# Kernel tuning notes

Hardware: AMD Instinct MI355X
Metric: run time of the kernel (lower is better)

## Reference

```python
import jax, jax.numpy as jnp
import numpy as np

W_BIT = 4
G_SIZE = 128
HID = 4096
INTER = 11008
TOKS = (2, 2048)


def _dequant(qw, qz, scales, g_size):
    """Unpack int4 nibbles from int32 and dequantize: (w - zero) * scale.
    qw: [K, N//8] int32, qz: [K//g, N//8] int32, scales: [K//g, N] float.
    Returns dense weight [K, N] in scales.dtype."""
    K = qw.shape[0]
    shifts = (jnp.arange(8, dtype=jnp.int32) * 4)  # 8 nibbles per int32
    w = ((qw[:, :, None] >> shifts) & 0xF).reshape(K, -1).astype(scales.dtype)   # [K, N]
    z = ((qz[:, :, None] >> shifts) & 0xF).reshape(qz.shape[0], -1).astype(scales.dtype)  # [K//g, N]
    zr = jnp.repeat(z, g_size, axis=0)       # broadcast zero-points over group rows
    sr = jnp.repeat(scales, g_size, axis=0)  # broadcast scales over group rows
    return (w - zr) * sr


def setup_inputs() -> dict:
    key = jax.random.key(0)
    ks = jax.random.split(key, 7)
    B, S = TOKS
    x = jax.random.normal(ks[0], (B, S, HID), dtype=jnp.float32)
    imax = 2147483647
    qweight_gu = jax.random.randint(ks[1], (HID, 2 * INTER // 8), 0, imax, dtype=jnp.int32)
    qzeros_gu = jax.random.randint(ks[2], (HID // G_SIZE, 2 * INTER // 8), 0, imax, dtype=jnp.int32)
    scales_gu = jax.random.uniform(ks[3], (HID // G_SIZE, 2 * INTER), dtype=jnp.float32) * 0.01 + 1e-3
    qweight_dn = jax.random.randint(ks[4], (INTER, HID // 8), 0, imax, dtype=jnp.int32)
    qzeros_dn = jax.random.randint(ks[5], (INTER // G_SIZE, HID // 8), 0, imax, dtype=jnp.int32)
    scales_dn = jax.random.uniform(ks[6], (INTER // G_SIZE, HID), dtype=jnp.float32) * 0.01 + 1e-3
    return {"x": x, "qweight_gu": qweight_gu, "qzeros_gu": qzeros_gu, "scales_gu": scales_gu,
            "qweight_dn": qweight_dn, "qzeros_dn": qzeros_dn, "scales_dn": scales_dn}


def reference(x, qweight_gu, qzeros_gu, scales_gu, qweight_dn, qzeros_dn, scales_dn):
    # gate_up projection: x [B,S,H] @ W_gu [H, 2*I]
    W_gu = _dequant(qweight_gu, qzeros_gu, scales_gu, G_SIZE)
    gate_up = jnp.einsum('bsh,hi->bsi', x, W_gu)
    d = gate_up.shape[-1] // 2
    # SiluAndMul: silu(gate) * up
    h = jax.nn.silu(gate_up[..., :d]) * gate_up[..., d:]
    # down projection: h [B,S,I] @ W_dn [I, H]
    W_dn = _dequant(qweight_dn, qzeros_dn, scales_dn, G_SIZE)
    return jnp.einsum('bsi,ih->bsh', h, W_dn)
```

## Files before the change

kernel.cpp:

```cpp
#include <hip/hip_runtime.h>
#include <hip/hip_bf16.h>
#include <hip/hip_fp16.h>
#include <cstdint>
#include <cstddef>

#define AS1 __attribute__((address_space(1)))
#define AS3 __attribute__((address_space(3)))

constexpr int HIDC   = 4096;
constexpr int INTERC = 11008;
constexpr int NTOKC  = 4096;

using f32x4 = __attribute__((ext_vector_type(4))) float;
using f16x8 = __attribute__((ext_vector_type(8))) _Float16;


__global__ void cvt_x_kernel(const float4* __restrict__ x, ushort4* __restrict__ xh, int n4) {
  int stride = gridDim.x * blockDim.x;
  for (int i = blockIdx.x * blockDim.x + threadIdx.x; i < n4; i += stride) {
    float4 v = x[i];
    ushort4 o;
    o.x = __builtin_bit_cast(unsigned short, __float2half(v.x));
    o.y = __builtin_bit_cast(unsigned short, __float2half(v.y));
    o.z = __builtin_bit_cast(unsigned short, __float2half(v.z));
    o.w = __builtin_bit_cast(unsigned short, __float2half(v.w));
    xh[i] = o;
  }
}

template <int GU>
__global__ void deq_kernel(const uint32_t* __restrict__ qw, const uint32_t* __restrict__ qz,
                           const float* __restrict__ sc, __half* __restrict__ WT,
                           int cbase, int K, int Wn8, int Nsc) {
  __shared__ __align__(16) __half tile[64][32];
  const int tid = threadIdx.x;
  const int bx = blockIdx.x;
  const int k0 = blockIdx.y * 32;
  const int k  = tid & 31, ws = tid >> 5;
  const int g  = (k0 + k) >> 7;
  int wordidx, nbase, nploc0;
  if (GU) {
    const int n0p = cbase + bx * 64;
    const int h0  = n0p >> 1;
    const int mat = ws >> 2, wsq = ws & 3;
    wordidx = (mat * INTERC + h0) / 8 + wsq;
    nbase   = mat * INTERC + h0 + wsq * 8;
    nploc0  = ((wsq >> 1) << 5) + mat * 16 + ((wsq & 1) << 3);
  } else {
    const int n0 = cbase + bx * 64;
    wordidx = n0 / 8 + ws;
    nbase   = n0 + ws * 8;
    nploc0  = ws * 8;
  }
  uint32_t q  = qw[(size_t)(k0 + k) * Wn8 + wordidx];
  uint32_t zw = qz[(size_t)g * Wn8 + wordidx];
#pragma unroll
  for (int j = 0; j < 8; ++j) {
    float v = (float)((q >> (4 * j)) & 0xFu);
    float z = (float)((zw >> (4 * j)) & 0xFu);
    float s = sc[(size_t)g * Nsc + nbase + j];
    tile[nploc0 + j][k] = __float2half((v - z) * s);
  }
  __syncthreads();
  const int nl = tid >> 2, kc = (tid & 3) * 8;
  uint4 vv = *(const uint4*)&tile[nl][kc];
  *(uint4*)&WT[(size_t)(bx * 64 + nl) * K + k0 + kc] = vv;
}

template <int DUAL, int NT, int K>
__global__ __launch_bounds__(512, 1) void qgemm_kernel(
    const __half* __restrict__ A, const __half* __restrict__ B,
    __half* __restrict__ Hout, float* __restrict__ Fout) {
  __shared__ __align__(16) char lds[131072];
  const int tid  = threadIdx.x;
  const int lane = tid & 63;
  const int w    = tid >> 6;
  const int wr   = w >> 2, wc = w & 3;
  const int fr   = lane & 15, fq = lane >> 4;

  const int nwg8 = (int)gridDim.x >> 3;
  const int g2   = ((int)blockIdx.x & 7) * nwg8 + ((int)blockIdx.x >> 3);
  const int nt   = g2 >> 4;
  const int mt   = g2 & 15;
  const int row0 = mt * 256, col0 = nt * 256;

  int a_src[4], b_src[4];
#pragma unroll
  for (int i = 0; i < 4; ++i) {
    int o = i * 8192 + tid * 16;
    int r = o >> 7;
    int b = (o & 127) ^ ((r & 7) << 4);
    a_src[i] = (row0 + r) * K + (b >> 1);
    b_src[i] = (col0 + r) * K + (b >> 1);
  }

  f32x4 acc[8][4] = {};
  f16x8 av[4], bv0[4], bv1[4];

  auto glA = [&](int i, int kt, int buf) {
    __builtin_amdgcn_global_load_lds(
        (const AS1 uint32_t*)(A + (size_t)a_src[i] + (size_t)kt * 64),
        (AS3 uint32_t*)(lds + buf * 65536 + i * 8192 + w * 1024), 16, 0, 0);
  };
  auto glB = [&](int i, int kt, int buf) {
    __builtin_amdgcn_global_load_lds(
        (const AS1 uint32_t*)(B + (size_t)b_src[i] + (size_t)kt * 64),
        (AS3 uint32_t*)(lds + buf * 65536 + 32768 + i * 8192 + w * 1024), 16, 0, 0);
  };
  auto rdA = [&](int buf, int mh, int kk) {
    const int bb = (((kk << 2) | fq) ^ (fr & 7)) << 4;
    const char* base = lds + buf * 65536;
#pragma unroll
    for (int j = 0; j < 4; ++j)
      av[j] = *(const f16x8*)(base + (wr * 128 + mh * 64 + j * 16 + fr) * 128 + bb);
  };
  auto rdB = [&](int buf, int kk, f16x8* dst) {
    const int bb = (((kk << 2) | fq) ^ (fr & 7)) << 4;
    const char* base = lds + buf * 65536 + 32768;
#pragma unroll
    for (int n = 0; n < 4; ++n)
      dst[n] = *(const f16x8*)(base + (wc * 64 + n * 16 + fr) * 128 + bb);
  };
  auto mfma16 = [&](f16x8* bvp, int mh) {
    __builtin_amdgcn_s_setprio(1);
#pragma unroll
    for (int j = 0; j < 4; ++j)
#pragma unroll
      for (int n = 0; n < 4; ++n)
        acc[mh * 4 + j][n] =
            __builtin_amdgcn_mfma_f32_16x16x32_f16(av[j], bvp[n], acc[mh * 4 + j][n], 0, 0, 0);
    __builtin_amdgcn_s_setprio(0);
  };

  glB(0, 0, 0); glB(1, 0, 0); glB(2, 0, 0); glB(3, 0, 0);
  glA(0, 0, 0); glA(2, 0, 0); glA(1, 0, 0); glA(3, 0, 0);
  asm volatile("s_waitcnt vmcnt(2)" ::: "memory");
  asm volatile("s_barrier" ::: "memory");

#pragma unroll 1
  for (int kt = 0; kt < NT; ++kt) {
    const int cur = kt & 1, nxt = cur ^ 1;
    const bool stg = (kt + 1 < NT);
    if (stg) { glB(0, kt + 1, nxt); glB(1, kt + 1, nxt); }
    rdB(cur, 0, bv0);
    rdA(cur, 0, 0);
    mfma16(bv0, 0);
    if (stg) { glB(2, kt + 1, nxt); glB(3, kt + 1, nxt); }
    rdB(cur, 1, bv1);
    rdA(cur, 0, 1);
    mfma16(bv1, 0);
    if (stg) asm volatile("s_waitcnt vmcnt(4)" ::: "memory");
    else     asm volatile("s_waitcnt vmcnt(0)" ::: "memory");
    asm volatile("s_barrier" ::: "memory");
    if (stg) { glA(0, kt + 1, nxt); glA(2, kt + 1, nxt); }
    rdA(cur, 1, 0);
    mfma16(bv0, 1);
    if (stg) { glA(1, kt + 1, nxt); glA(3, kt + 1, nxt); }
    rdA(cur, 1, 1);
    mfma16(bv1, 1);
    if (stg) asm volatile("s_waitcnt vmcnt(2)" ::: "memory");
    asm volatile("s_barrier" ::: "memory");
  }

  if (DUAL) {
#pragma unroll
    for (int mi = 0; mi < 8; ++mi) {
      const int rr = row0 + wr * 128 + mi * 16 + fq * 4;
#pragma unroll
      for (int pp = 0; pp < 2; ++pp) {
        const int hcol = nt * 128 + (wc * 2 + pp) * 16 + fr;
#pragma unroll
        for (int r = 0; r < 4; ++r) {
          float gv = acc[mi][2 * pp][r];
          float uv = acc[mi][2 * pp + 1][r];
          float hv = gv / (1.0f + __expf(-gv)) * uv;
          Hout[(size_t)(rr + r) * INTERC + hcol] = __float2half(hv);
        }
      }
    }
  } else {
#pragma unroll
    for (int mi = 0; mi < 8; ++mi) {
      const int rr = row0 + wr * 128 + mi * 16 + fq * 4;
#pragma unroll
      for (int ni = 0; ni < 4; ++ni) {
        const int cc = nt * 256 + wc * 64 + ni * 16 + fr;
#pragma unroll
        for (int r = 0; r < 4; ++r)
          Fout[(size_t)(rr + r) * HIDC + cc] = acc[mi][ni][r];
      }
    }
  }
}

extern "C" void kernel_launch(void* const* d_in, const int* in_sizes, int n_in,
                              void* d_out, int out_size, void* d_ws, size_t ws_size,
                              hipStream_t stream) {
  const float*    x     = (const float*)d_in[0];
  const uint32_t* qw_gu = (const uint32_t*)d_in[1];
  const uint32_t* qz_gu = (const uint32_t*)d_in[2];
  const float*    sc_gu = (const float*)d_in[3];
  const uint32_t* qw_dn = (const uint32_t*)d_in[4];
  const uint32_t* qz_dn = (const uint32_t*)d_in[5];
  const float*    sc_dn = (const float*)d_in[6];
  float* out = (float*)d_out;

  char* ws = (char*)d_ws;
  __half* xh   = (__half*)(ws);
  __half* WT   = (__half*)(ws + 33554432);
  __half* hbuf = (__half*)(ws + 100663296);
  __half* WTdn = (__half*)(ws);

  cvt_x_kernel<<<2048, 256, 0, stream>>>((const float4*)x, (ushort4*)xh, NTOKC * HIDC / 4);

  const int cb[3] = {0, 8192, 16384};
  const int nc[3] = {8192, 8192, 5632};
  for (int c = 0; c < 3; ++c) {
    deq_kernel<1><<<dim3(nc[c] / 64, HIDC / 32), 256, 0, stream>>>(
        qw_gu, qz_gu, sc_gu, WT, cb[c], HIDC, 2752, 22016);
    qgemm_kernel<1, 64, HIDC><<<(nc[c] / 256) * 16, 512, 0, stream>>>(
        xh, WT, hbuf + cb[c] / 2, nullptr);
  }

  deq_kernel<0><<<dim3(HIDC / 64, INTERC / 32), 256, 0, stream>>>(
      qw_dn, qz_dn, sc_dn, WTdn, 0, INTERC, 512, HIDC);
  qgemm_kernel<0, 172, INTERC><<<(HIDC / 256) * 16, 512, 0, stream>>>(
      hbuf, WTdn, nullptr, out);
}
```

Measured before the change: 1.097 ms.

## Switch GEMM to 32x32x16 MFMA with single-barrier K-loop pipeline

Replaces the 16x16x32 f16 MFMA tiling with 32x32x16 MFMA tiles (4x2 per wave), and changes the LDS fragment reads and swizzle indexing to match. The dequant tile layout for gate/up is rearranged so each 32-column block pairs gate and up for the SiLU epilogue. The K loop now runs four k-slices with one full vmcnt(0) wait and one barrier per iteration instead of two partial waits and two barriers. The intent is fewer LDS reads per FLOP and higher MFMA throughput, at the cost of less overlap, since each iteration now waits for all outstanding loads.

```diff
diff --git a/kernel.cpp b/kernel.cpp
--- a/kernel.cpp
+++ b/kernel.cpp
@@ -11,8 +11,8 @@
 constexpr int INTERC = 11008;
 constexpr int NTOKC  = 4096;
 
-using f32x4 = __attribute__((ext_vector_type(4))) float;
-using f16x8 = __attribute__((ext_vector_type(8))) _Float16;
+using f32x16 = __attribute__((ext_vector_type(16))) float;
+using f16x8  = __attribute__((ext_vector_type(8))) _Float16;
 
 
 __global__ void cvt_x_kernel(const float4* __restrict__ x, ushort4* __restrict__ xh, int n4) {
@@ -45,7 +45,7 @@
     const int mat = ws >> 2, wsq = ws & 3;
     wordidx = (mat * INTERC + h0) / 8 + wsq;
     nbase   = mat * INTERC + h0 + wsq * 8;
-    nploc0  = ((wsq >> 1) << 5) + mat * 16 + ((wsq & 1) << 3);
+    nploc0  = mat * 32 + wsq * 8;
   } else {
     const int n0 = cbase + bx * 64;
     wordidx = n0 / 8 + ws;
@@ -76,7 +76,9 @@
   const int lane = tid & 63;
   const int w    = tid >> 6;
   const int wr   = w >> 2, wc = w & 3;
-  const int fr   = lane & 15, fq = lane >> 4;
+  const int fr   = lane & 31;
+  const int khf  = lane >> 5;
+  const int l7   = lane & 7;
 
   const int nwg8 = (int)gridDim.x >> 3;
   const int g2   = ((int)blockIdx.x & 7) * nwg8 + ((int)blockIdx.x >> 3);
@@ -94,8 +96,7 @@
     b_src[i] = (col0 + r) * K + (b >> 1);
   }
 
-  f32x4 acc[8][4] = {};
-  f16x8 av[4], bv0[4], bv1[4];
+  f32x16 acc[4][2] = {};
 
   auto glA = [&](int i, int kt, int buf) {
     __builtin_amdgcn_global_load_lds(
@@ -107,87 +108,72 @@
         (const AS1 uint32_t*)(B + (size_t)b_src[i] + (size_t)kt * 64),
         (AS3 uint32_t*)(lds + buf * 65536 + 32768 + i * 8192 + w * 1024), 16, 0, 0);
   };
-  auto rdA = [&](int buf, int mh, int kk) {
-    const int bb = (((kk << 2) | fq) ^ (fr & 7)) << 4;
+
+  auto slice = [&](int buf, int s) {
+    const int bb = (((s << 1) | khf) ^ l7) << 4;
     const char* base = lds + buf * 65536;
-#pragma unroll
-    for (int j = 0; j < 4; ++j)
-      av[j] = *(const f16x8*)(base + (wr * 128 + mh * 64 + j * 16 + fr) * 128 + bb);
-  };
-  auto rdB = [&](int buf, int kk, f16x8* dst) {
-    const int bb = (((kk << 2) | fq) ^ (fr & 7)) << 4;
-    const char* base = lds + buf * 65536 + 32768;
-#pragma unroll
-    for (int n = 0; n < 4; ++n)
-      dst[n] = *(const f16x8*)(base + (wc * 64 + n * 16 + fr) * 128 + bb);
-  };
-  auto mfma16 = [&](f16x8* bvp, int mh) {
+    f16x8 av[4], bv[2];
+#pragma unroll
+    for (int m = 0; m < 4; ++m)
+      av[m] = *(const f16x8*)(base + (wr * 128 + m * 32 + fr) * 128 + bb);
+#pragma unroll
+    for (int n = 0; n < 2; ++n)
+      bv[n] = *(const f16x8*)(base + 32768 + (wc * 64 + n * 32 + fr) * 128 + bb);
     __builtin_amdgcn_s_setprio(1);
 #pragma unroll
-    for (int j = 0; j < 4; ++j)
-#pragma unroll
-      for (int n = 0; n < 4; ++n)
-        acc[mh * 4 + j][n] =
-            __builtin_amdgcn_mfma_f32_16x16x32_f16(av[j], bvp[n], acc[mh * 4 + j][n], 0, 0, 0);
+    for (int m = 0; m < 4; ++m)
+#pragma unroll
+      for (int n = 0; n < 2; ++n)
+        acc[m][n] = __builtin_amdgcn_mfma_f32_32x32x16_f16(av[m], bv[n], acc[m][n], 0, 0, 0);
     __builtin_amdgcn_s_setprio(0);
   };
 
   glB(0, 0, 0); glB(1, 0, 0); glB(2, 0, 0); glB(3, 0, 0);
   glA(0, 0, 0); glA(2, 0, 0); glA(1, 0, 0); glA(3, 0, 0);
-  asm volatile("s_waitcnt vmcnt(2)" ::: "memory");
+  asm volatile("s_waitcnt vmcnt(0)" ::: "memory");
   asm volatile("s_barrier" ::: "memory");
 
 #pragma unroll 1
   for (int kt = 0; kt < NT; ++kt) {
     const int cur = kt & 1, nxt = cur ^ 1;
     const bool stg = (kt + 1 < NT);
-    if (stg) { glB(0, kt + 1, nxt); glB(1, kt + 1, nxt); }
-    rdB(cur, 0, bv0);
-    rdA(cur, 0, 0);
-    mfma16(bv0, 0);
-    if (stg) { glB(2, kt + 1, nxt); glB(3, kt + 1, nxt); }
-    rdB(cur, 1, bv1);
-    rdA(cur, 0, 1);
-    mfma16(bv1, 0);
-    if (stg) asm volatile("s_waitcnt vmcnt(4)" ::: "memory");
-    else     asm volatile("s_waitcnt vmcnt(0)" ::: "memory");
+    if (stg) { glB(0, kt + 1, nxt); glB(1, kt + 1, nxt); glB(2, kt + 1, nxt); glB(3, kt + 1, nxt); }
+    slice(cur, 0);
+    if (stg) { glA(0, kt + 1, nxt); glA(2, kt + 1, nxt); }
+    slice(cur, 1);
+    if (stg) { glA(1, kt + 1, nxt); glA(3, kt + 1, nxt); }
+    slice(cur, 2);
+    slice(cur, 3);
+    asm volatile("s_waitcnt vmcnt(0)" ::: "memory");
     asm volatile("s_barrier" ::: "memory");
-    if (stg) { glA(0, kt + 1, nxt); glA(2, kt + 1, nxt); }
-    rdA(cur, 1, 0);
-    mfma16(bv0, 1);
-    if (stg) { glA(1, kt + 1, nxt); glA(3, kt + 1, nxt); }
-    rdA(cur, 1, 1);
-    mfma16(bv1, 1);
-    if (stg) asm volatile("s_waitcnt vmcnt(2)" ::: "memory");
-    asm volatile("s_barrier" ::: "memory");
   }
 
   if (DUAL) {
-#pragma unroll
-    for (int mi = 0; mi < 8; ++mi) {
-      const int rr = row0 + wr * 128 + mi * 16 + fq * 4;
-#pragma unroll
-      for (int pp = 0; pp < 2; ++pp) {
-        const int hcol = nt * 128 + (wc * 2 + pp) * 16 + fr;
-#pragma unroll
-        for (int r = 0; r < 4; ++r) {
-          float gv = acc[mi][2 * pp][r];
-          float uv = acc[mi][2 * pp + 1][r];
-          float hv = gv / (1.0f + __expf(-gv)) * uv;
-          Hout[(size_t)(rr + r) * INTERC + hcol] = __float2half(hv);
-        }
+    const int hcol = nt * 128 + wc * 32 + fr;
+#pragma unroll
+    for (int m = 0; m < 4; ++m) {
+      const int rbase = row0 + wr * 128 + m * 32 + khf * 4;
+#pragma unroll
+      for (int r = 0; r < 16; ++r) {
+        const int row = rbase + (r & 3) + ((r >> 2) << 3);
+        float gv = acc[m][0][r];
+        float uv = acc[m][1][r];
+        float hv = gv / (1.0f + __expf(-gv)) * uv;
+        Hout[(size_t)row * INTERC + hcol] = __float2half(hv);
       }
     }
   } else {
 #pragma unroll
-    for (int mi = 0; mi < 8; ++mi) {
-      const int rr = row0 + wr * 128 + mi * 16 + fq * 4;
-#pragma unroll
-      for (int ni = 0; ni < 4; ++ni) {
-        const int cc = nt * 256 + wc * 64 + ni * 16 + fr;
-#pragma unroll
-        for (int r = 0; r < 4; ++r)
-          Fout[(size_t)(rr + r) * HIDC + cc] = acc[mi][ni][r];
+    for (int m = 0; m < 4; ++m) {
+      const int rbase = row0 + wr * 128 + m * 32 + khf * 4;
+#pragma unroll
+      for (int n = 0; n < 2; ++n) {
+        const int cc = nt * 256 + wc * 64 + n * 32 + fr;
+#pragma unroll
+        for (int r = 0; r < 16; ++r) {
+          const int row = rbase + (r & 3) + ((r >> 2) << 3);
+          Fout[(size_t)row * HIDC + cc] = acc[m][n][r];
+        }
       }
     }
   }
```

New measurement: 1.283 ms. 1.17x slower.

## Fuse next-chunk weight dequant into gate-up GEMM blocks with double-buffered weights

Applied to the files above, without the earlier changes.

The gate_up projection is split into six column chunks. Each GEMM launch also dequantizes the next chunk's int4 weights into a second ping-pong buffer, done by the first few blocks before they start their GEMM work. This removes the separate dequant launches and aims to overlap dequantization with GEMM execution. In exchange, the dequant blocks finish their GEMM tiles late, there are more, smaller GEMM launches, and a second weight buffer occupies workspace.

```diff
diff --git a/kernel.cpp b/kernel.cpp
--- a/kernel.cpp
+++ b/kernel.cpp
@@ -67,19 +67,58 @@
   *(uint4*)&WT[(size_t)(bx * 64 + nl) * K + k0 + kc] = vv;
 }
 
-template <int DUAL, int NT, int K>
-__global__ __launch_bounds__(512, 1) void qgemm_kernel(
-    const __half* __restrict__ A, const __half* __restrict__ B,
-    __half* __restrict__ Hout, float* __restrict__ Fout) {
+__global__ __launch_bounds__(512, 1) void g1f_kernel(
+    const __half* __restrict__ A, const __half* __restrict__ Bcur,
+    __half* __restrict__ Hout,
+    const uint32_t* __restrict__ qw, const uint32_t* __restrict__ qz,
+    const float* __restrict__ sc, __half* __restrict__ Bnext,
+    int cb_next, int ndq, int ng) {
   __shared__ __align__(16) char lds[131072];
   const int tid  = threadIdx.x;
+  const int bid  = blockIdx.x;
+
+  if (bid < ndq) {
+    __half* tile = (__half*)lds;
+    const int pg  = cb_next + bid * 16;
+    const int mat = (pg >> 4) & 1;
+    const int hcb = (pg >> 5) << 4;
+    const int cw  = tid >> 8;
+    const int k   = tid & 255;
+    const int wordidx = mat * (INTERC / 8) + (hcb >> 3) + cw;
+#pragma unroll 1
+    for (int it = 0; it < HIDC / 256; ++it) {
+      const int kk = it * 256 + k;
+      const int g  = kk >> 7;
+      uint32_t q  = qw[(size_t)kk * (2 * INTERC / 8) + wordidx];
+      uint32_t zw = qz[(size_t)g * (2 * INTERC / 8) + wordidx];
+      const float* sp = sc + (size_t)g * (2 * INTERC) + mat * INTERC + hcb + cw * 8;
+      float4 s0 = *(const float4*)sp;
+      float4 s1 = *(const float4*)(sp + 4);
+      float ss[8] = {s0.x, s0.y, s0.z, s0.w, s1.x, s1.y, s1.z, s1.w};
+#pragma unroll
+      for (int j = 0; j < 8; ++j) {
+        float v = (float)((q >> (4 * j)) & 0xFu);
+        float z = (float)((zw >> (4 * j)) & 0xFu);
+        tile[(cw * 8 + j) * 256 + k] = __float2half((v - z) * ss[j]);
+      }
+      __syncthreads();
+      const int nl = tid >> 5, kc = (tid & 31) * 8;
+      uint4 vv = *(const uint4*)&tile[nl * 256 + kc];
+      *(uint4*)&Bnext[(size_t)(bid * 16 + nl) * HIDC + it * 256 + kc] = vv;
+      __syncthreads();
+    }
+  }
+  __syncthreads();
+
+  constexpr int NT = HIDC / 64;
+  constexpr int K  = HIDC;
   const int lane = tid & 63;
   const int w    = tid >> 6;
   const int wr   = w >> 2, wc = w & 3;
   const int fr   = lane & 15, fq = lane >> 4;
 
-  const int nwg8 = (int)gridDim.x >> 3;
-  const int g2   = ((int)blockIdx.x & 7) * nwg8 + ((int)blockIdx.x >> 3);
+  const int nwg8 = ng >> 3;
+  const int g2   = (bid & 7) * nwg8 + (bid >> 3);
   const int nt   = g2 >> 4;
   const int mt   = g2 & 15;
   const int row0 = mt * 256, col0 = nt * 256;
@@ -104,7 +143,7 @@
   };
   auto glB = [&](int i, int kt, int buf) {
     __builtin_amdgcn_global_load_lds(
-        (const AS1 uint32_t*)(B + (size_t)b_src[i] + (size_t)kt * 64),
+        (const AS1 uint32_t*)(Bcur + (size_t)b_src[i] + (size_t)kt * 64),
         (AS3 uint32_t*)(lds + buf * 65536 + 32768 + i * 8192 + w * 1024), 16, 0, 0);
   };
   auto rdA = [&](int buf, int mh, int kk) {
@@ -162,33 +201,127 @@
     asm volatile("s_barrier" ::: "memory");
   }
 
-  if (DUAL) {
-#pragma unroll
-    for (int mi = 0; mi < 8; ++mi) {
-      const int rr = row0 + wr * 128 + mi * 16 + fq * 4;
-#pragma unroll
-      for (int pp = 0; pp < 2; ++pp) {
-        const int hcol = nt * 128 + (wc * 2 + pp) * 16 + fr;
-#pragma unroll
-        for (int r = 0; r < 4; ++r) {
-          float gv = acc[mi][2 * pp][r];
-          float uv = acc[mi][2 * pp + 1][r];
-          float hv = gv / (1.0f + __expf(-gv)) * uv;
-          Hout[(size_t)(rr + r) * INTERC + hcol] = __float2half(hv);
-        }
+#pragma unroll
+  for (int mi = 0; mi < 8; ++mi) {
+    const int rr = row0 + wr * 128 + mi * 16 + fq * 4;
+#pragma unroll
+    for (int pp = 0; pp < 2; ++pp) {
+      const int hcol = nt * 128 + (wc * 2 + pp) * 16 + fr;
+#pragma unroll
+      for (int r = 0; r < 4; ++r) {
+        float gv = acc[mi][2 * pp][r];
+        float uv = acc[mi][2 * pp + 1][r];
+        float hv = gv / (1.0f + __expf(-gv)) * uv;
+        Hout[(size_t)(rr + r) * INTERC + hcol] = __float2half(hv);
       }
     }
-  } else {
-#pragma unroll
-    for (int mi = 0; mi < 8; ++mi) {
-      const int rr = row0 + wr * 128 + mi * 16 + fq * 4;
-#pragma unroll
-      for (int ni = 0; ni < 4; ++ni) {
-        const int cc = nt * 256 + wc * 64 + ni * 16 + fr;
-#pragma unroll
-        for (int r = 0; r < 4; ++r)
-          Fout[(size_t)(rr + r) * HIDC + cc] = acc[mi][ni][r];
-      }
+  }
+}
+
+template <int NT, int K>
+__global__ __launch_bounds__(512, 1) void qgemm_kernel(
+    const __half* __restrict__ A, const __half* __restrict__ B,
+    float* __restrict__ Fout) {
+  __shared__ __align__(16) char lds[131072];
+  const int tid  = threadIdx.x;
+  const int lane = tid & 63;
+  const int w    = tid >> 6;
+  const int wr   = w >> 2, wc = w & 3;
+  const int fr   = lane & 15, fq = lane >> 4;
+
+  const int nwg8 = (int)gridDim.x >> 3;
+  const int g2   = ((int)blockIdx.x & 7) * nwg8 + ((int)blockIdx.x >> 3);
+  const int nt   = g2 >> 4;
+  const int mt   = g2 & 15;
+  const int row0 = mt * 256, col0 = nt * 256;
+
+  int a_src[4], b_src[4];
+#pragma unroll
+  for (int i = 0; i < 4; ++i) {
+    int o = i * 8192 + tid * 16;
+    int r = o >> 7;
+    int b = (o & 127) ^ ((r & 7) << 4);
+    a_src[i] = (row0 + r) * K + (b >> 1);
+    b_src[i] = (col0 + r) * K + (b >> 1);
+  }
+
+  f32x4 acc[8][4] = {};
+  f16x8 av[4], bv0[4], bv1[4];
+
+  auto glA = [&](int i, int kt, int buf) {
+    __builtin_amdgcn_global_load_lds(
+        (const AS1 uint32_t*)(A + (size_t)a_src[i] + (size_t)kt * 64),
+        (AS3 uint32_t*)(lds + buf * 65536 + i * 8192 + w * 1024), 16, 0, 0);
+  };
+  auto glB = [&](int i, int kt, int buf) {
+    __builtin_amdgcn_global_load_lds(
+        (const AS1 uint32_t*)(B + (size_t)b_src[i] + (size_t)kt * 64),
+        (AS3 uint32_t*)(lds + buf * 65536 + 32768 + i * 8192 + w * 1024), 16, 0, 0);
+  };
+  auto rdA = [&](int buf, int mh, int kk) {
+    const int bb = (((kk << 2) | fq) ^ (fr & 7)) << 4;
+    const char* base = lds + buf * 65536;
+#pragma unroll
+    for (int j = 0; j < 4; ++j)
+      av[j] = *(const f16x8*)(base + (wr * 128 + mh * 64 + j * 16 + fr) * 128 + bb);
+  };
+  auto rdB = [&](int buf, int kk, f16x8* dst) {
+    const int bb = (((kk << 2) | fq) ^ (fr & 7)) << 4;
+    const char* base = lds + buf * 65536 + 32768;
+#pragma unroll
+    for (int n = 0; n < 4; ++n)
+      dst[n] = *(const f16x8*)(base + (wc * 64 + n * 16 + fr) * 128 + bb);
+  };
+  auto mfma16 = [&](f16x8* bvp, int mh) {
+    __builtin_amdgcn_s_setprio(1);
+#pragma unroll
+    for (int j = 0; j < 4; ++j)
+#pragma unroll
+      for (int n = 0; n < 4; ++n)
+        acc[mh * 4 + j][n] =
+            __builtin_amdgcn_mfma_f32_16x16x32_f16(av[j], bvp[n], acc[mh * 4 + j][n], 0, 0, 0);
+    __builtin_amdgcn_s_setprio(0);
+  };
+
+  glB(0, 0, 0); glB(1, 0, 0); glB(2, 0, 0); glB(3, 0, 0);
+  glA(0, 0, 0); glA(2, 0, 0); glA(1, 0, 0); glA(3, 0, 0);
+  asm volatile("s_waitcnt vmcnt(2)" ::: "memory");
+  asm volatile("s_barrier" ::: "memory");
+
+#pragma unroll 1
+  for (int kt = 0; kt < NT; ++kt) {
+    const int cur = kt & 1, nxt = cur ^ 1;
+    const bool stg = (kt + 1 < NT);
+    if (stg) { glB(0, kt + 1, nxt); glB(1, kt + 1, nxt); }
+    rdB(cur, 0, bv0);
+    rdA(cur, 0, 0);
+    mfma16(bv0, 0);
+    if (stg) { glB(2, kt + 1, nxt); glB(3, kt + 1, nxt); }
+    rdB(cur, 1, bv1);
+    rdA(cur, 0, 1);
+    mfma16(bv1, 0);
+    if (stg) asm volatile("s_waitcnt vmcnt(4)" ::: "memory");
+    else     asm volatile("s_waitcnt vmcnt(0)" ::: "memory");
+    asm volatile("s_barrier" ::: "memory");
+    if (stg) { glA(0, kt + 1, nxt); glA(2, kt + 1, nxt); }
+    rdA(cur, 1, 0);
+    mfma16(bv0, 1);
+    if (stg) { glA(1, kt + 1, nxt); glA(3, kt + 1, nxt); }
+    rdA(cur, 1, 1);
+    mfma16(bv1, 1);
+    if (stg) asm volatile("s_waitcnt vmcnt(2)" ::: "memory");
+    asm volatile("s_barrier" ::: "memory");
+  }
+
+#pragma unroll
+  for (int mi = 0; mi < 8; ++mi) {
+    const int rr = row0 + wr * 128 + mi * 16 + fq * 4;
+#pragma unroll
+    for (int ni = 0; ni < 4; ++ni) {
+      const int cc = nt * 256 + wc * 64 + ni * 16 + fr;
+#pragma unroll
+      for (int r = 0; r < 4; ++r)
+        Fout[(size_t)(rr + r) * HIDC + cc] = acc[mi][ni][r];
     }
   }
 }
@@ -206,24 +339,27 @@
   float* out = (float*)d_out;
 
   char* ws = (char*)d_ws;
-  __half* xh   = (__half*)(ws);
-  __half* WT   = (__half*)(ws + 33554432);
-  __half* hbuf = (__half*)(ws + 100663296);
-  __half* WTdn = (__half*)(ws);
+  __half* xh    = (__half*)(ws);
+  __half* WTs[2] = {(__half*)(ws + 33554432), (__half*)(ws + 67108864)};
+  __half* hbuf  = (__half*)(ws + 100663296);
+  __half* WTdn  = (__half*)(ws);
 
   cvt_x_kernel<<<2048, 256, 0, stream>>>((const float4*)x, (ushort4*)xh, NTOKC * HIDC / 4);
-
-  const int cb[3] = {0, 8192, 16384};
-  const int nc[3] = {8192, 8192, 5632};
-  for (int c = 0; c < 3; ++c) {
-    deq_kernel<1><<<dim3(nc[c] / 64, HIDC / 32), 256, 0, stream>>>(
-        qw_gu, qz_gu, sc_gu, WT, cb[c], HIDC, 2752, 22016);
-    qgemm_kernel<1, 64, HIDC><<<(nc[c] / 256) * 16, 512, 0, stream>>>(
-        xh, WT, hbuf + cb[c] / 2, nullptr);
+  deq_kernel<1><<<dim3(64, 128), 256, 0, stream>>>(
+      qw_gu, qz_gu, sc_gu, WTs[0], 0, HIDC, 2 * INTERC / 8, 2 * INTERC);
+
+  const int cbs[7] = {0, 4096, 8192, 12288, 16384, 20480, 22016};
+  for (int k = 0; k < 6; ++k) {
+    const int nc  = cbs[k + 1] - cbs[k];
+    const int ng  = (nc / 256) * 16;
+    const int ncn = (k < 5) ? (cbs[k + 2] - cbs[k + 1]) : 0;
+    const int ndq = ncn / 16;
+    g1f_kernel<<<ng, 512, 0, stream>>>(
+        xh, WTs[k & 1], hbuf + cbs[k] / 2,
+        qw_gu, qz_gu, sc_gu, WTs[(k + 1) & 1], cbs[k + 1], ndq, ng);
   }
 
   deq_kernel<0><<<dim3(HIDC / 64, INTERC / 32), 256, 0, stream>>>(
-      qw_dn, qz_dn, sc_dn, WTdn, 0, INTERC, 512, HIDC);
-  qgemm_kernel<0, 172, INTERC><<<(HIDC / 256) * 16, 512, 0, stream>>>(
-      hbuf, WTdn, nullptr, out);
-}
+      qw_dn, qz_dn, sc_dn, WTdn, 0, INTERC, HIDC / 8, HIDC);
+  qgemm_kernel<172, INTERC><<<(HIDC / 256) * 16, 512, 0, stream>>>(hbuf, WTdn, out);
+}
```

After: 1.147 ms. 4.6% more time.
